# Performance work log

Measured on AMD Instinct MI355X. Metric: run time of the kernel, lower is better.

## Reference

```python
import jax, jax.numpy as jnp
import numpy as np

N = 12288
D = 16


def setup_inputs() -> dict:
    key = jax.random.key(0)
    k_a, k_u1, k_u2 = jax.random.split(key, 3)
    # 0/1 directed adjacency matrix (dense, as nx.to_numpy_array produces)
    A = jax.random.randint(k_a, (N, N), 0, 2).astype(jnp.float32)
    # tf.random.uniform init for the factor matrices
    U1 = jax.random.uniform(k_u1, (N, D), dtype=jnp.float32)
    U2 = jax.random.uniform(k_u2, (N, D), dtype=jnp.float32)
    lmbd1 = jnp.float32(0.01)
    return {"A": A, "U1": U1, "U2": U2, "lmbd1": lmbd1}


def reference(A, U1, U2, lmbd1):
    # scores[i,j] = <U1[i], U2[j]>  -> full N x N materialization (hot path)
    scores = U1 @ U2.T  # [N, N]
    # original: log(1 / (1 + exp(-scores))) == log_sigmoid(scores)
    loss = -jnp.sum(A * jax.nn.log_sigmoid(scores))
    # L1 regularization: sum over lmbd1*(|U1| + |U2|) elementwise
    loss = loss + lmbd1 * (jnp.sum(jnp.abs(U1)) + jnp.sum(jnp.abs(U2)))
    return loss
```

## Files before the change

### kernel.cpp

```cpp
#include <hip/hip_runtime.h>

#define N_DIM 12288
#define D_DIM 16
#define TILE_R 256
#define TILE_C 128
#define GROUP  4

typedef float f2 __attribute__((ext_vector_type(2)));
typedef float f4 __attribute__((ext_vector_type(4)));

__global__ void zero_kernel(float* __restrict__ out) {
    out[0] = 0.0f;
}

__global__ void l1_kernel(const float* __restrict__ U1,
                          const float* __restrict__ U2,
                          const float* __restrict__ lmbd,
                          float* __restrict__ out) {
    const int M = N_DIM * D_DIM;
    int idx = blockIdx.x * blockDim.x + threadIdx.x;
    int stride = gridDim.x * blockDim.x;
    float s = 0.0f;
    for (int i = idx; i < M; i += stride)
        s += fabsf(U1[i]) + fabsf(U2[i]);
    #pragma unroll
    for (int off = 32; off; off >>= 1)
        s += __shfl_down(s, off, 64);
    __shared__ float ws[4];
    int lane = threadIdx.x & 63;
    int wave = threadIdx.x >> 6;
    if (lane == 0) ws[wave] = s;
    __syncthreads();
    if (threadIdx.x == 0)
        atomicAdd(out, lmbd[0] * (ws[0] + ws[1] + ws[2] + ws[3]));
}

__global__ __launch_bounds__(256, 6)
void loss_kernel(const float* __restrict__ A,
                 const float* __restrict__ U1,
                 const float* __restrict__ U2,
                 float* __restrict__ out) {
    const int t    = threadIdx.x;
    const int lane = t & 63;
    const int wave = t >> 6;
    const int r0   = blockIdx.y * TILE_R;
    const int c0   = blockIdx.x * TILE_C;

    __shared__ float u1s[TILE_R * D_DIM];

    {
        const f4* src = (const f4*)U1 + (size_t)r0 * (D_DIM / 4);
        f4* dst = (f4*)u1s;
        #pragma unroll
        for (int i = 0; i < (TILE_R * D_DIM / 4) / 256; ++i)
            dst[i * 256 + t] = src[i * 256 + t];
    }

    float u2r[2][D_DIM];
    #pragma unroll
    for (int j = 0; j < 2; ++j) {
        const f4* p = (const f4*)(U2 + (size_t)(c0 + lane * 2 + j) * D_DIM);
        f4 qa = p[0], qb = p[1], qc = p[2], qd = p[3];
        u2r[j][0]  = qa.x; u2r[j][1]  = qa.y; u2r[j][2]  = qa.z; u2r[j][3]  = qa.w;
        u2r[j][4]  = qb.x; u2r[j][5]  = qb.y; u2r[j][6]  = qb.z; u2r[j][7]  = qb.w;
        u2r[j][8]  = qc.x; u2r[j][9]  = qc.y; u2r[j][10] = qc.z; u2r[j][11] = qc.w;
        u2r[j][12] = qd.x; u2r[j][13] = qd.y; u2r[j][14] = qd.z; u2r[j][15] = qd.w;
    }

    __syncthreads();

    const int wr0 = wave * 64;
    const float* __restrict__ ap =
        A + (size_t)(r0 + wr0) * N_DIM + (size_t)c0 + lane * 2;

    const float L2E = 1.4426950408889634f;
    float acc = 0.0f;

    for (int g = 0; g < 64 / GROUP; ++g) {
        f2 av[GROUP];
        #pragma unroll
        for (int r = 0; r < GROUP; ++r)
            av[r] = __builtin_nontemporal_load(
                        (const f2*)(ap + (size_t)r * N_DIM));

        float p0 = 1.0f, p1 = 1.0f;
        #pragma unroll
        for (int r = 0; r < GROUP; ++r) {
            const f4* uq = (const f4*)(u1s + (wr0 + g * GROUP + r) * D_DIM);
            f4 qa = uq[0], qb = uq[1], qc = uq[2], qd = uq[3];
            float u1v[D_DIM];
            u1v[0]  = qa.x; u1v[1]  = qa.y; u1v[2]  = qa.z; u1v[3]  = qa.w;
            u1v[4]  = qb.x; u1v[5]  = qb.y; u1v[6]  = qb.z; u1v[7]  = qb.w;
            u1v[8]  = qc.x; u1v[9]  = qc.y; u1v[10] = qc.z; u1v[11] = qc.w;
            u1v[12] = qd.x; u1v[13] = qd.y; u1v[14] = qd.z; u1v[15] = qd.w;

            float s0 = 0.0f, s1 = 0.0f;
            #pragma unroll
            for (int k = 0; k < D_DIM; ++k) {
                s0 = fmaf(u1v[k], u2r[0][k], s0);
                s1 = fmaf(u1v[k], u2r[1][k], s1);
            }
            float e0 = __builtin_amdgcn_exp2f(-L2E * s0);
            float e1 = __builtin_amdgcn_exp2f(-L2E * s1);
            p0 *= fmaf(av[r].x, e0, 1.0f);
            p1 *= fmaf(av[r].y, e1, 1.0f);
        }
        acc += __builtin_amdgcn_logf(p0 * p1);
        ap += (size_t)GROUP * N_DIM;
    }

    float part = acc * 0.69314718055994531f;

    #pragma unroll
    for (int off = 32; off; off >>= 1)
        part += __shfl_down(part, off, 64);
    __shared__ float wsum[4];
    if (lane == 0) wsum[wave] = part;
    __syncthreads();
    if (t == 0)
        atomicAdd(out, wsum[0] + wsum[1] + wsum[2] + wsum[3]);
}

extern "C" void kernel_launch(void* const* d_in, const int* in_sizes, int n_in,
                              void* d_out, int out_size, void* d_ws, size_t ws_size,
                              hipStream_t stream) {
    const float* A    = (const float*)d_in[0];
    const float* U1   = (const float*)d_in[1];
    const float* U2   = (const float*)d_in[2];
    const float* lmbd = (const float*)d_in[3];
    float* out = (float*)d_out;

    zero_kernel<<<1, 64, 0, stream>>>(out);
    l1_kernel<<<256, 256, 0, stream>>>(U1, U2, lmbd, out);

    dim3 grid(N_DIM / TILE_C, N_DIM / TILE_R);
    loss_kernel<<<grid, 256, 0, stream>>>(A, U1, U2, out);
}
```

Baseline: 753.0 us.

## Double-buffer A row loads with software pipelining and larger groups

Replaces the per-group load-then-compute loop with a double-buffered software pipeline: the next group of A rows is loaded into a second register buffer while the current group is computed. The group size goes from 4 to 8 rows (fewer log calls per row) and the occupancy hint drops from 6 to 4 blocks per CU to make room for the extra registers. The aim is to hide HBM latency on the streaming A reads, at the cost of lower occupancy and higher register pressure.

```diff
diff --git a/kernel.cpp b/kernel.cpp
--- a/kernel.cpp
+++ b/kernel.cpp
@@ -4,7 +4,7 @@
 #define D_DIM 16
 #define TILE_R 256
 #define TILE_C 128
-#define GROUP  4
+#define GRP    8
 
 typedef float f2 __attribute__((ext_vector_type(2)));
 typedef float f4 __attribute__((ext_vector_type(4)));
@@ -35,7 +35,7 @@
         atomicAdd(out, lmbd[0] * (ws[0] + ws[1] + ws[2] + ws[3]));
 }
 
-__global__ __launch_bounds__(256, 6)
+__global__ __launch_bounds__(256, 4)
 void loss_kernel(const float* __restrict__ A,
                  const float* __restrict__ U1,
                  const float* __restrict__ U2,
@@ -76,38 +76,46 @@
     const float L2E = 1.4426950408889634f;
     float acc = 0.0f;
 
-    for (int g = 0; g < 64 / GROUP; ++g) {
-        f2 av[GROUP];
-        #pragma unroll
-        for (int r = 0; r < GROUP; ++r)
-            av[r] = __builtin_nontemporal_load(
-                        (const f2*)(ap + (size_t)r * N_DIM));
+    f2 av[GRP], bv[GRP];
 
-        float p0 = 1.0f, p1 = 1.0f;
-        #pragma unroll
-        for (int r = 0; r < GROUP; ++r) {
-            const f4* uq = (const f4*)(u1s + (wr0 + g * GROUP + r) * D_DIM);
-            f4 qa = uq[0], qb = uq[1], qc = uq[2], qd = uq[3];
-            float u1v[D_DIM];
-            u1v[0]  = qa.x; u1v[1]  = qa.y; u1v[2]  = qa.z; u1v[3]  = qa.w;
-            u1v[4]  = qb.x; u1v[5]  = qb.y; u1v[6]  = qb.z; u1v[7]  = qb.w;
-            u1v[8]  = qc.x; u1v[9]  = qc.y; u1v[10] = qc.z; u1v[11] = qc.w;
-            u1v[12] = qd.x; u1v[13] = qd.y; u1v[14] = qd.z; u1v[15] = qd.w;
+#define LOADG(buf, g)                                                         \
+    { _Pragma("unroll")                                                       \
+      for (int r = 0; r < GRP; ++r)                                           \
+          buf[r] = __builtin_nontemporal_load(                                \
+              (const f2*)(ap + (size_t)((g) * GRP + r) * N_DIM)); }
 
-            float s0 = 0.0f, s1 = 0.0f;
-            #pragma unroll
-            for (int k = 0; k < D_DIM; ++k) {
-                s0 = fmaf(u1v[k], u2r[0][k], s0);
-                s1 = fmaf(u1v[k], u2r[1][k], s1);
-            }
-            float e0 = __builtin_amdgcn_exp2f(-L2E * s0);
-            float e1 = __builtin_amdgcn_exp2f(-L2E * s1);
-            p0 *= fmaf(av[r].x, e0, 1.0f);
-            p1 *= fmaf(av[r].y, e1, 1.0f);
-        }
-        acc += __builtin_amdgcn_logf(p0 * p1);
-        ap += (size_t)GROUP * N_DIM;
+#define COMPG(buf, g)                                                         \
+    { float p0 = 1.0f, p1 = 1.0f;                                             \
+      _Pragma("unroll")                                                       \
+      for (int r = 0; r < GRP; ++r) {                                         \
+          const f4* uq = (const f4*)(u1s + (wr0 + (g) * GRP + r) * D_DIM);    \
+          f4 qa = uq[0], qb = uq[1], qc = uq[2], qd = uq[3];                  \
+          float u1v[D_DIM] = {qa.x, qa.y, qa.z, qa.w, qb.x, qb.y, qb.z, qb.w, \
+                              qc.x, qc.y, qc.z, qc.w, qd.x, qd.y, qd.z, qd.w};\
+          float s0 = 0.0f, s1 = 0.0f;                                         \
+          _Pragma("unroll")                                                   \
+          for (int k = 0; k < D_DIM; ++k) {                                   \
+              s0 = fmaf(u1v[k], u2r[0][k], s0);                               \
+              s1 = fmaf(u1v[k], u2r[1][k], s1);                               \
+          }                                                                   \
+          float e0 = __builtin_amdgcn_exp2f(-L2E * s0);                       \
+          float e1 = __builtin_amdgcn_exp2f(-L2E * s1);                       \
+          p0 *= fmaf(buf[r].x, e0, 1.0f);                                     \
+          p1 *= fmaf(buf[r].y, e1, 1.0f);                                     \
+      }                                                                       \
+      acc += __builtin_amdgcn_logf(p0 * p1); }
+
+    LOADG(av, 0);
+    #pragma unroll
+    for (int gg = 0; gg < (64 / GRP) / 2; ++gg) {
+        LOADG(bv, 2 * gg + 1);
+        COMPG(av, 2 * gg);
+        if (2 * gg + 2 < 64 / GRP)
+            LOADG(av, 2 * gg + 2);
+        COMPG(bv, 2 * gg + 1);
     }
+#undef LOADG
+#undef COMPG
 
     float part = acc * 0.69314718055994531f;
 
```

New measurement: 743.2 us. Within noise of the previous version (-1.3%).
